# Kernel tuning notes

Hardware: AMD Instinct MI355X
Metric: run time of the kernel (lower is better)

Reference implementation:

```python
import jax, jax.numpy as jnp
import numpy as np

N_MODULES = 8
FIELDS_PER_MOD = 8
PARAMS_PER_FIELD = 8
AMOUNT_NODES = 65536
R = 1024
P_TOTAL = N_MODULES * FIELDS_PER_MOD * PARAMS_PER_FIELD  # 512 params in DB


def setup_inputs() -> dict:
    key = jax.random.key(0)
    k1, k2, k3 = jax.random.split(key, 3)
    # Flat scaled DB buffer: every param tiled over AMOUNT_NODES (AXIS==0 path of build_db).
    db = jax.random.normal(k1, (P_TOTAL * AMOUNT_NODES,), dtype=jnp.float32)
    # Structural index tables (constants driving get_db_index prefix sums).
    fields = jnp.full((N_MODULES,), FIELDS_PER_MOD, dtype=jnp.int32)
    params_per_field = jnp.full((N_MODULES * FIELDS_PER_MOD,), PARAMS_PER_FIELD, dtype=jnp.int32)
    scaled_params = jnp.full((P_TOTAL,), AMOUNT_NODES, dtype=jnp.int32)
    # method_to_db: (mod_idx, field_idx, param_in_field_idx) triples.
    coords = jnp.stack([
        jax.random.randint(k2, (R,), 0, N_MODULES),
        jax.random.randint(jax.random.fold_in(k2, 1), (R,), 0, FIELDS_PER_MOD),
        jax.random.randint(jax.random.fold_in(k2, 2), (R,), 0, PARAMS_PER_FIELD),
    ], axis=1).astype(jnp.int32)
    # step_results: one node-grid block per coordinate triple.
    results = jax.random.normal(k3, (R, AMOUNT_NODES), dtype=jnp.float32)
    return {"db": db, "results": results, "fields": fields,
            "params_per_field": params_per_field,
            "scaled_params": scaled_params, "coords": coords}


def _exclusive_prefix(x):
    return jnp.concatenate([jnp.zeros((1,), x.dtype), jnp.cumsum(x)])


def _db_starts(fields, params_per_field, scaled_params, coords):
    # get_db_index: relative (mod, field, param) -> scaled flat start index.
    pf = _exclusive_prefix(fields)            # fields before module m
    pp = _exclusive_prefix(params_per_field)  # params before abs field
    ps = _exclusive_prefix(scaled_params)     # scaled elems before abs param
    abs_field = pf[coords[:, 0]] + coords[:, 1]
    abs_param = pp[abs_field] + coords[:, 2]
    return ps[abs_param]                      # [R]


def reference(db, results, fields, params_per_field, scaled_params, coords):
    starts = _db_starts(fields, params_per_field, scaled_params, coords)  # [R]
    blk = results.shape[1]  # uniform scaled param length (= amount_nodes)
    # get_parameter_vector / extract_field_param_variation: batched dynamic slices.
    gathered = jax.vmap(lambda s: jax.lax.dynamic_slice_in_dim(db, s, blk))(starts)  # [R, blk]
    # sort_results / scatter_results_to_db: write result blocks back into DB.
    idx = starts[:, None] + jnp.arange(blk, dtype=starts.dtype)  # [R, blk] flat indices
    new_db = db.at[idx.reshape(-1)].set(results.reshape(-1))
    return gathered, new_db
```

## Files before the change

### kernel.cpp

```cpp
#include <hip/hip_runtime.h>

__global__ void compute_starts_kernel(const int* __restrict__ fields,
                                      const int* __restrict__ ppf,
                                      const int* __restrict__ sp,
                                      const int* __restrict__ coords,
                                      int R, int P_TOTAL,
                                      int* __restrict__ starts,
                                      int* __restrict__ owner) {
    int tid = threadIdx.x;
    for (int p = tid; p < P_TOTAL; p += blockDim.x) owner[p] = -1;
    __syncthreads();
    for (int r = tid; r < R; r += blockDim.x) {
        int mod   = coords[3 * r + 0];
        int field = coords[3 * r + 1];
        int par   = coords[3 * r + 2];
        int pf = 0;
        for (int m = 0; m < mod; ++m) pf += fields[m];
        int abs_field = pf + field;
        int pp = 0;
        for (int f = 0; f < abs_field; ++f) pp += ppf[f];
        int abs_param = pp + par;
        int ps = 0;
        for (int q = 0; q < abs_param; ++q) ps += sp[q];
        starts[r] = ps;
        atomicMax(&owner[abs_param], r);
    }
}

__global__ void gather_kernel(const float4* __restrict__ db,
                              const int* __restrict__ starts,
                              float4* __restrict__ out,
                              int blk4) {
    int r = blockIdx.y;
    int j = blockIdx.x * blockDim.x + threadIdx.x;
    if (j >= blk4) return;
    int s4 = starts[r] >> 2;
    out[(long long)r * blk4 + j] = db[s4 + j];
}

__global__ void scatter_merge_kernel(const float4* __restrict__ db,
                                     const float4* __restrict__ results,
                                     const int* __restrict__ owner,
                                     float4* __restrict__ newdb,
                                     int blk4) {
    int p = blockIdx.y;
    int j = blockIdx.x * blockDim.x + threadIdx.x;
    if (j >= blk4) return;
    long long i = (long long)p * blk4 + j;
    int r = owner[p];
    newdb[i] = (r >= 0) ? results[(long long)r * blk4 + j] : db[i];
}

extern "C" void kernel_launch(void* const* d_in, const int* in_sizes, int n_in,
                              void* d_out, int out_size, void* d_ws, size_t ws_size,
                              hipStream_t stream) {
    const float* db      = (const float*)d_in[0];
    const float* results = (const float*)d_in[1];
    const int* fields    = (const int*)d_in[2];
    const int* ppf       = (const int*)d_in[3];
    const int* sp        = (const int*)d_in[4];
    const int* coords    = (const int*)d_in[5];

    const int db_size = in_sizes[0];
    const int R       = in_sizes[5] / 3;
    const int blk     = in_sizes[1] / R;
    const int P_TOTAL = in_sizes[4];

    int* starts = (int*)d_ws;
    int* owner  = starts + R;

    compute_starts_kernel<<<1, 1024, 0, stream>>>(fields, ppf, sp, coords,
                                                  R, P_TOTAL, starts, owner);

    const int blk4 = blk / 4;
    const int bx = (blk4 + 255) / 256;

    dim3 ggrid(bx, R);
    gather_kernel<<<ggrid, 256, 0, stream>>>((const float4*)db, starts,
                                             (float4*)d_out, blk4);

    float4* newdb = (float4*)d_out + (long long)R * blk4;
    dim3 sgrid(bx, P_TOTAL);
    scatter_merge_kernel<<<sgrid, 256, 0, stream>>>((const float4*)db,
                                                    (const float4*)results,
                                                    owner, newdb, blk4);
}
```

Measured before the change: 635.6 us.

## Fuse gather and scatter-merge kernels, LDS prefix scans, nontemporal vector copies

Replaces the per-thread serial prefix-sum loops in the index kernel with LDS exclusive scans. Merges the gather and scatter-merge kernels into one launch whose grid rows cover both the R gathered blocks and the P_TOTAL db blocks. Each thread now copies four float4 values and uses nontemporal loads and stores to keep streaming data out of cache. The LDS scans assume fixed maximum table sizes and that the scan length fits within the 1024-thread block.

```diff
diff --git a/kernel.cpp b/kernel.cpp
--- a/kernel.cpp
+++ b/kernel.cpp
@@ -1,54 +1,99 @@
 #include <hip/hip_runtime.h>
+
+typedef float v4f __attribute__((ext_vector_type(4)));
+
+
+#define PF_MAX 256
+#define PP_MAX 1024
+#define PS_MAX 2048
+
+__device__ __forceinline__ void excl_scan_lds(int* s, int n, int t) {
+    int orig = (t < n) ? s[t] : 0;
+    for (int off = 1; off < n; off <<= 1) {
+        int v = (t < n && t >= off) ? s[t - off] : 0;
+        __syncthreads();
+        if (t < n) s[t] += v;
+        __syncthreads();
+    }
+    if (t < n) s[t] -= orig;
+    __syncthreads();
+}
 
 __global__ void compute_starts_kernel(const int* __restrict__ fields,
                                       const int* __restrict__ ppf,
                                       const int* __restrict__ sp,
                                       const int* __restrict__ coords,
-                                      int R, int P_TOTAL,
+                                      int NF, int NPF, int R, int P_TOTAL,
                                       int* __restrict__ starts,
                                       int* __restrict__ owner) {
-    int tid = threadIdx.x;
-    for (int p = tid; p < P_TOTAL; p += blockDim.x) owner[p] = -1;
+    __shared__ int s_pf[PF_MAX];
+    __shared__ int s_pp[PP_MAX];
+    __shared__ int s_ps[PS_MAX];
+    const int t = threadIdx.x;
+
+    if (t < NF && t < PF_MAX)  s_pf[t] = fields[t];
+    if (t < NPF && t < PP_MAX) s_pp[t] = ppf[t];
+    for (int q = t; q < P_TOTAL && q < PS_MAX; q += blockDim.x) s_ps[q] = sp[q];
+    for (int p = t; p < P_TOTAL; p += blockDim.x) owner[p] = -1;
     __syncthreads();
-    for (int r = tid; r < R; r += blockDim.x) {
+
+    excl_scan_lds(s_pf, NF, t);
+    excl_scan_lds(s_pp, NPF, t);
+    excl_scan_lds(s_ps, P_TOTAL, t);
+
+    for (int r = t; r < R; r += blockDim.x) {
         int mod   = coords[3 * r + 0];
         int field = coords[3 * r + 1];
         int par   = coords[3 * r + 2];
-        int pf = 0;
-        for (int m = 0; m < mod; ++m) pf += fields[m];
-        int abs_field = pf + field;
-        int pp = 0;
-        for (int f = 0; f < abs_field; ++f) pp += ppf[f];
-        int abs_param = pp + par;
-        int ps = 0;
-        for (int q = 0; q < abs_param; ++q) ps += sp[q];
-        starts[r] = ps;
+        int abs_field = s_pf[mod] + field;
+        int abs_param = s_pp[abs_field] + par;
+        starts[r] = s_ps[abs_param];
         atomicMax(&owner[abs_param], r);
     }
 }
 
-__global__ void gather_kernel(const float4* __restrict__ db,
-                              const int* __restrict__ starts,
-                              float4* __restrict__ out,
-                              int blk4) {
-    int r = blockIdx.y;
-    int j = blockIdx.x * blockDim.x + threadIdx.x;
-    if (j >= blk4) return;
-    int s4 = starts[r] >> 2;
-    out[(long long)r * blk4 + j] = db[s4 + j];
-}
+#define VEC 4
 
-__global__ void scatter_merge_kernel(const float4* __restrict__ db,
-                                     const float4* __restrict__ results,
+__global__ void fused_gather_scatter(const v4f* __restrict__ db,
+                                     const v4f* __restrict__ results,
+                                     const int* __restrict__ starts,
                                      const int* __restrict__ owner,
-                                     float4* __restrict__ newdb,
-                                     int blk4) {
-    int p = blockIdx.y;
-    int j = blockIdx.x * blockDim.x + threadIdx.x;
-    if (j >= blk4) return;
-    long long i = (long long)p * blk4 + j;
-    int r = owner[p];
-    newdb[i] = (r >= 0) ? results[(long long)r * blk4 + j] : db[i];
+                                     v4f* __restrict__ gathered,
+                                     v4f* __restrict__ newdb,
+                                     int R, int blk4) {
+    const int row = blockIdx.y;
+    const int j0  = blockIdx.x * (blockDim.x * VEC) + threadIdx.x;
+
+    if (row < R) {
+        const int s4 = starts[row] >> 2;
+        v4f* dst = gathered + (long long)row * blk4;
+#pragma unroll
+        for (int k = 0; k < VEC; ++k) {
+            int j = j0 + k * (int)blockDim.x;
+            if (j < blk4) __builtin_nontemporal_store(db[s4 + j], &dst[j]);
+        }
+    } else {
+        const int p = row - R;
+        const int r = owner[p];
+        const long long base = (long long)p * blk4;
+        v4f* dst = newdb + base;
+        if (r >= 0) {
+            const v4f* src = results + (long long)r * blk4;
+#pragma unroll
+            for (int k = 0; k < VEC; ++k) {
+                int j = j0 + k * (int)blockDim.x;
+                if (j < blk4)
+                    __builtin_nontemporal_store(__builtin_nontemporal_load(&src[j]), &dst[j]);
+            }
+        } else {
+            const v4f* src = db + base;
+#pragma unroll
+            for (int k = 0; k < VEC; ++k) {
+                int j = j0 + k * (int)blockDim.x;
+                if (j < blk4) __builtin_nontemporal_store(src[j], &dst[j]);
+            }
+        }
+    }
 }
 
 extern "C" void kernel_launch(void* const* d_in, const int* in_sizes, int n_in,
@@ -61,7 +106,8 @@
     const int* sp        = (const int*)d_in[4];
     const int* coords    = (const int*)d_in[5];
 
-    const int db_size = in_sizes[0];
+    const int NF      = in_sizes[2];
+    const int NPF     = in_sizes[3];
     const int R       = in_sizes[5] / 3;
     const int blk     = in_sizes[1] / R;
     const int P_TOTAL = in_sizes[4];
@@ -70,18 +116,20 @@
     int* owner  = starts + R;
 
     compute_starts_kernel<<<1, 1024, 0, stream>>>(fields, ppf, sp, coords,
-                                                  R, P_TOTAL, starts, owner);
+                                                  NF, NPF, R, P_TOTAL,
+                                                  starts, owner);
 
     const int blk4 = blk / 4;
-    const int bx = (blk4 + 255) / 256;
+    const int per_wg = 256 * VEC;
+    const int gx = (blk4 + per_wg - 1) / per_wg;
 
-    dim3 ggrid(bx, R);
-    gather_kernel<<<ggrid, 256, 0, stream>>>((const float4*)db, starts,
-                                             (float4*)d_out, blk4);
+    v4f* gathered = (v4f*)d_out;
+    v4f* newdb    = gathered + (long long)R * blk4;
 
-    float4* newdb = (float4*)d_out + (long long)R * blk4;
-    dim3 sgrid(bx, P_TOTAL);
-    scatter_merge_kernel<<<sgrid, 256, 0, stream>>>((const float4*)db,
-                                                    (const float4*)results,
-                                                    owner, newdb, blk4);
+    dim3 grid(gx, R + P_TOTAL);
+    fused_gather_scatter<<<grid, 256, 0, stream>>>((const v4f*)db,
+                                                   (const v4f*)results,
+                                                   starts, owner,
+                                                   gathered, newdb,
+                                                   R, blk4);
 }
```

Measured after the change: 619.7 us. 1.03x faster.
